# Performance work log

Hardware: AMD Instinct MI355X
Metric: run time of the kernel (lower is better)

## Reference

```python
import jax, jax.numpy as jnp
import numpy as np

# ---- box encoding helpers ----

def _cv2_corners(b):
    # b: [..., 5] (cx, cy, w, h, angle) -> [..., 4, 2] rotated-rect vertices
    cx, cy, w, h, a = (b[..., i] for i in range(5))
    c, s = jnp.cos(a), jnp.sin(a)
    dx, dy = w * 0.5, h * 0.5
    lx = jnp.stack([-dx, dx, dx, -dx], axis=-1)   # [..., 4]
    ly = jnp.stack([-dy, -dy, dy, dy], axis=-1)
    x = cx[..., None] + lx * c[..., None] - ly * s[..., None]
    y = cy[..., None] + lx * s[..., None] + ly * c[..., None]
    return jnp.stack([x, y], axis=-1)


def _vertices_to_cv2(v):
    # v: [..., 4, 2] ordered vertices -> [..., 5] (cx, cy, w, h, angle)
    ctr = v.mean(axis=-2)
    e1 = v[..., 1, :] - v[..., 0, :]
    e2 = v[..., 3, :] - v[..., 0, :]
    w = jnp.linalg.norm(e1, axis=-1)
    h = jnp.linalg.norm(e2, axis=-1)
    ang = jnp.arctan2(e1[..., 1], e1[..., 0])
    return jnp.concatenate([ctr, w[..., None], h[..., None], ang[..., None]], axis=-1)


def _corners_to_hbb(corners):
    # [..., 4, 2] -> [..., 4] (x1, y1, x2, y2)
    return jnp.concatenate([corners.min(axis=-2), corners.max(axis=-2)], axis=-1)


def _box_iou(a, b):
    # a: [B, N, 4], b: [B, M, 4] -> [B, N, M] axis-aligned IoU
    lt = jnp.maximum(a[:, :, None, :2], b[:, None, :, :2])
    rb = jnp.minimum(a[:, :, None, 2:], b[:, None, :, 2:])
    wh = jnp.clip(rb - lt, 0.0)
    inter = wh[..., 0] * wh[..., 1]
    area_a = (a[..., 2] - a[..., 0]) * (a[..., 3] - a[..., 1])
    area_b = (b[..., 2] - b[..., 0]) * (b[..., 3] - b[..., 1])
    union = area_a[:, :, None] + area_b[:, None, :] - inter
    return inter / jnp.clip(union, 1e-7)


def setup_inputs() -> dict:
    key = jax.random.key(0)
    ks = jax.random.split(key, 6)
    B, N, M, C = 8, 16384, 128, 81

    def rand_boxes(k, shape):
        k1, k2, k3 = jax.random.split(k, 3)
        ctr = jax.random.uniform(k1, shape + (2,), minval=0.0, maxval=1000.0)
        wh = jax.random.uniform(k2, shape + (2,), minval=16.0, maxval=160.0)
        ang = jax.random.uniform(k3, shape + (1,), minval=-1.5, maxval=1.5)
        return jnp.concatenate([ctr, wh, ang], axis=-1)

    box_pred = rand_boxes(ks[0], (B, N))
    gt = rand_boxes(ks[1], (B, M))
    # seed the first M predictions near the GT so positives (IoU>=0.5) exist
    box_pred = box_pred.at[:, :M].set(gt + 2.0 * jax.random.normal(ks[2], gt.shape))
    regression_targets = _cv2_corners(gt)                     # [B, M, 4, 2] vertices
    classification_targets = jax.random.randint(ks[3], (B, M), 0, C - 1)
    class_pred = jax.random.normal(ks[4], (B, N, C))
    return {
        "box_pred": box_pred,
        "class_pred": class_pred,
        "regression_targets": regression_targets,
        "classification_targets": classification_targets,
        "n_samples": 256,
    }


def reference(box_pred, class_pred, regression_targets, classification_targets, n_samples):
    B = box_pred.shape[0]
    C = class_pred.shape[-1]
    background_cls = C - 1
    k_pos = n_samples // 2
    k_neg = n_samples - k_pos

    box_targets_cv2 = _vertices_to_cv2(regression_targets)           # [B, M, 5]
    hbb_pred = _corners_to_hbb(_cv2_corners(box_pred))               # [B, N, 4]
    hbb_tgt = _corners_to_hbb(regression_targets)                    # [B, M, 4]
    iou = _box_iou(hbb_pred, hbb_tgt)                                # [B, N, M]

    def per_image(iou_i, labels_i, logits_i, boxp_i, boxt_i):
        max_iou = iou_i.max(axis=-1)                                 # [N]
        match = iou_i.argmax(axis=-1)                                # [N] matched GT idx
        pos_mask = max_iou >= 0.5
        # sample up to k_pos positives (highest IoU) and k_neg negatives (lowest IoU)
        pos_score = jnp.where(pos_mask, max_iou, -1.0)
        _, pos_idx = jax.lax.top_k(pos_score, k_pos)
        pos_valid = pos_mask[pos_idx]
        neg_score = jnp.where(pos_mask, -jnp.inf, -max_iou)
        _, neg_idx = jax.lax.top_k(neg_score, k_neg)
        neg_valid = ~pos_mask[neg_idx]
        # classification targets: matched GT label for positives, background otherwise
        cls_target = jnp.where(pos_mask, labels_i[match], background_cls)
        sel_idx = jnp.concatenate([pos_idx, neg_idx])                # [n_samples]
        sel_valid = jnp.concatenate([pos_valid, neg_valid])
        logp = jax.nn.log_softmax(logits_i[sel_idx], axis=-1)        # [n_samples, C]
        nll = -jnp.take_along_axis(logp, cls_target[sel_idx][:, None], axis=1)[:, 0]
        cls_loss = jnp.sum(nll * sel_valid.astype(logp.dtype))
        rel_pred = boxp_i[pos_idx]                                   # [k_pos, 5]
        rel_gt = boxt_i[match[pos_idx]]                              # [k_pos, 5]
        d = jnp.abs(rel_pred - rel_gt)
        sl1 = jnp.where(d < 1.0, 0.5 * d * d, d - 0.5)
        regr_loss = jnp.sum(sl1 * pos_valid[:, None].astype(sl1.dtype))
        return cls_loss, regr_loss

    cls_l, reg_l = jax.vmap(per_image)(
        iou, classification_targets, class_pred, box_pred, box_targets_cv2
    )
    classification_loss = cls_l.sum() / B
    regression_loss = reg_l.sum() / B
    total_loss = classification_loss + regression_loss
    return total_loss, classification_loss, regression_loss
```

## Files before the change

kernel.cpp:

```cpp
#include <hip/hip_runtime.h>
#include <math.h>

#define B_ 8
#define N_ 16384
#define M_ 128
#define C_ 81
#define TPB 512
#define KPT 32
#define NWAVE (TPB / 64)
#define ABLK 32
#define ATPB 512

__global__ __launch_bounds__(ATPB)
void iou_fused(const float* __restrict__ bp,
               const float* __restrict__ rt,
               unsigned* __restrict__ poskey,
               unsigned* __restrict__ negkey,
               unsigned char* __restrict__ match8,
               unsigned* __restrict__ cnt,
               float* __restrict__ out) {
    __shared__ float sx1[M_], sy1[M_], sx2[M_], sy2[M_], sab[M_];
    __shared__ unsigned scnt[ATPB / 64];
    int b = blockIdx.y;
    int n = blockIdx.x * ATPB + threadIdx.x;

    if (blockIdx.x == 0 && blockIdx.y == 0 && threadIdx.x < 3)
        out[threadIdx.x] = 0.0f;

    if (threadIdx.x < M_) {
        const float* v = rt + ((size_t)b * M_ + threadIdx.x) * 8;
        float x0 = v[0], y0 = v[1], x1 = v[2], y1 = v[3];
        float x2 = v[4], y2 = v[5], x3 = v[6], y3 = v[7];
        float mnx = fminf(fminf(x0, x1), fminf(x2, x3));
        float mny = fminf(fminf(y0, y1), fminf(y2, y3));
        float mxx = fmaxf(fmaxf(x0, x1), fmaxf(x2, x3));
        float mxy = fmaxf(fmaxf(y0, y1), fmaxf(y2, y3));
        sx1[threadIdx.x] = mnx; sy1[threadIdx.x] = mny;
        sx2[threadIdx.x] = mxx; sy2[threadIdx.x] = mxy;
        sab[threadIdx.x] = (mxx - mnx) * (mxy - mny);
    }
    __syncthreads();

    const float* p = bp + ((size_t)b * N_ + n) * 5;
    float cx = p[0], cy = p[1], w = p[2], h = p[3], a = p[4];
    float c = cosf(a), s = sinf(a);
    float dx = w * 0.5f, dy = h * 0.5f;
    float ex = fabsf(dx * c) + fabsf(dy * s);
    float ey = fabsf(dx * s) + fabsf(dy * c);
    float ax1 = cx - ex, ay1 = cy - ey, ax2 = cx + ex, ay2 = cy + ey;
    float area_a = (ax2 - ax1) * (ay2 - ay1);

    float bin = -1.0f, bun = 1.0f;
    int bm = 0;
#pragma unroll 4
    for (int m = 0; m < M_; m++) {
        float lx = fmaxf(ax1, sx1[m]), ly = fmaxf(ay1, sy1[m]);
        float rx = fminf(ax2, sx2[m]), ry = fminf(ay2, sy2[m]);
        float ww = fmaxf(rx - lx, 0.0f), hh = fmaxf(ry - ly, 0.0f);
        float inter = ww * hh;
        float uni = area_a + sab[m] - inter;
        bool better = inter * bun > bin * uni;
        bin = better ? inter : bin;
        bun = better ? uni : bun;
        bm = better ? m : bm;
    }
    float iou = bin / bun;
    unsigned bits = __float_as_uint(iou);
    bool pos = (iou >= 0.5f);
    size_t gi = (size_t)b * N_ + n;
    poskey[gi] = pos ? ~(bits | 0x80000000u) : 0xFFFFFFFFu;
    negkey[gi] = pos ? 0xFFFFFFFFu : (bits | 0x80000000u);
    match8[gi] = (unsigned char)bm;

    unsigned posb = (unsigned)__popcll(__ballot(pos));
    unsigned zerb = (unsigned)__popcll(__ballot(bits == 0u));
    int lane = threadIdx.x & 63, wv = threadIdx.x >> 6;
    if (lane == 0) scnt[wv] = posb | (zerb << 16);
    __syncthreads();
    if (threadIdx.x == 0) {
        unsigned t = 0;
#pragma unroll
        for (int i = 0; i < ATPB / 64; i++) t += scnt[i];
        cnt[(size_t)b * ABLK + blockIdx.x] = t;
    }
}

__device__ __forceinline__ unsigned wave_sum6(unsigned c) {
    unsigned s = 0;
#pragma unroll
    for (int bit = 0; bit < 6; bit++)
        s += (unsigned)__popcll(__ballot((c >> bit) & 1u)) << bit;
    return s;
}

__device__ __forceinline__ unsigned bsum(unsigned c, unsigned* slot) {
    unsigned ws = wave_sum6(c);
    if ((threadIdx.x & 63) == 0) slot[threadIdx.x >> 6] = ws;
    __syncthreads();
    unsigned r = 0;
#pragma unroll
    for (int i = 0; i < NWAVE; i++) r += slot[i];
    return r;
}

__global__ __launch_bounds__(TPB)
void select_loss(const unsigned* __restrict__ keys_pos,
                 const unsigned* __restrict__ keys_neg,
                 const unsigned char* __restrict__ match8,
                 const float* __restrict__ logits, const float* __restrict__ bp,
                 const float* __restrict__ rt, const int* __restrict__ labels,
                 const int* __restrict__ ns_ptr, const unsigned* __restrict__ cnt,
                 float* __restrict__ out) {
    int type = blockIdx.x;
    int b = blockIdx.y;
    __shared__ float s_cv2[5][M_];
    __shared__ unsigned red[2 * NWAVE] __attribute__((aligned(16)));
    __shared__ float fredc[NWAVE], fredr[NWAVE];
    __shared__ unsigned sel[256];
    __shared__ unsigned selcnt;
    __shared__ unsigned s_tot;

    int tid = threadIdx.x;
    int lane = tid & 63, wv = tid >> 6;
    if (tid == 0) selcnt = 0;

    const unsigned* kb = (type == 0) ? keys_pos : keys_neg;
    const uint4* k4 = (const uint4*)(kb + (size_t)b * N_);
    uint4 kv[KPT / 4];
#pragma unroll
    for (int q = 0; q < KPT / 4; q++) kv[q] = k4[tid * (KPT / 4) + q];

    if (type == 0 && tid < M_) {
        const float* v = rt + ((size_t)b * M_ + tid) * 8;
        float x0 = v[0], y0 = v[1], x1 = v[2], y1 = v[3];
        float x2 = v[4], y2 = v[5], x3 = v[6], y3 = v[7];
        s_cv2[0][tid] = (x0 + x1 + x2 + x3) * 0.25f;
        s_cv2[1][tid] = (y0 + y1 + y2 + y3) * 0.25f;
        float e1x = x1 - x0, e1y = y1 - y0;
        float e2x = x3 - x0, e2y = y3 - y0;
        s_cv2[2][tid] = sqrtf(e1x * e1x + e1y * e1y);
        s_cv2[3][tid] = sqrtf(e2x * e2x + e2y * e2y);
        s_cv2[4][tid] = atan2f(e1y, e1x);
    }

    if (wv == 0) {
        unsigned c = (lane < ABLK) ? cnt[(size_t)b * ABLK + lane] : 0u;
#pragma unroll
        for (int o = 1; o < 64; o <<= 1) c += __shfl_xor(c, o);
        if (lane == 0) s_tot = c;
    }

    int ns = ns_ptr[0];
    unsigned ktar = (type == 0) ? (unsigned)(ns / 2) : (unsigned)(ns - ns / 2);
    if (ktar > 256u) ktar = 256u;

    unsigned key[KPT];
#pragma unroll
    for (int q = 0; q < KPT / 4; q++) {
        key[q * 4 + 0] = kv[q].x; key[q * 4 + 1] = kv[q].y;
        key[q * 4 + 2] = kv[q].z; key[q * 4 + 3] = kv[q].w;
    }
    int base = tid * KPT;

    __syncthreads();

    unsigned tot = s_tot;
    unsigned pos_total = tot & 0xFFFFu;
    unsigned zero_total = tot >> 16;
    unsigned V = (type == 0) ? pos_total : (unsigned)N_ - pos_total;
    unsigned keff = (ktar < V) ? ktar : V;

    int pc = 0;
    if (keff == V) {
#pragma unroll
        for (int j = 0; j < KPT; j++) {
            if (key[j] != 0xFFFFFFFFu) {
                unsigned p = atomicAdd(&selcnt, 1u);
                sel[p] = (unsigned)(base + j);
            }
        }
    } else {
        unsigned Ckey, m;
        bool zshort = (type == 1) && (zero_total >= keff);
        if (zshort) {
            Ckey = 0x80000000u;
            m = 0u;
        } else {
            unsigned lo = (type == 0) ? 0x40000000u : 0x80000000u;
            unsigned hi = (type == 0) ? 0x41000000u : 0xC0000000u;
            while (lo < hi) {
                unsigned mid = lo + ((hi - lo) >> 1);
                unsigned c = 0;
#pragma unroll
                for (int j = 0; j < KPT; j++) c += (key[j] <= mid) ? 1u : 0u;
                unsigned t2 = bsum(c, red + NWAVE * ((pc++) & 1));
                if (t2 >= keff) hi = mid; else lo = mid + 1;
            }
            Ckey = lo;
            unsigned cl = 0;
#pragma unroll
            for (int j = 0; j < KPT; j++) cl += (key[j] < Ckey) ? 1u : 0u;
            m = bsum(cl, red + NWAVE * ((pc++) & 1));
        }
        unsigned e = keff - m;

        unsigned ce = 0;
#pragma unroll
        for (int j = 0; j < KPT; j++) ce += (key[j] == Ckey) ? 1u : 0u;

        unsigned sc = ce;
#pragma unroll
        for (int o = 1; o < 64; o <<= 1) {
            unsigned t = __shfl_up(sc, o);
            if (lane >= o) sc += t;
        }
        unsigned* slot = red + NWAVE * ((pc++) & 1);
        if (lane == 63) slot[wv] = sc;
        __syncthreads();
        unsigned off = 0;
        for (int i = 0; i < wv; i++) off += slot[i];
        unsigned rank = off + sc - ce;

#pragma unroll
        for (int j = 0; j < KPT; j++) {
            unsigned k = key[j];
            bool s = false;
            if (k < Ckey) s = true;
            else if (k == Ckey) { s = (rank < e); rank++; }
            if (s) {
                unsigned p = atomicAdd(&selcnt, 1u);
                sel[p] = (unsigned)(base + j);
            }
        }
    }
    __syncthreads();
    unsigned total_sel = selcnt;

    float cls_sum = 0.f, reg_sum = 0.f;
    int q = tid & 3;
    for (unsigned sm = (unsigned)(tid >> 2); sm < total_sel; sm += TPB / 4) {
        unsigned i = sel[sm];
        const float* row = logits + ((size_t)b * N_ + i) * C_;
        int c0 = q * 21;
        int c1 = (c0 + 21 < C_) ? c0 + 21 : C_;
        float mx = -INFINITY;
        for (int c = c0; c < c1; c++) mx = fmaxf(mx, row[c]);
        mx = fmaxf(mx, __shfl_xor(mx, 1));
        mx = fmaxf(mx, __shfl_xor(mx, 2));
        float se = 0.f;
        for (int c = c0; c < c1; c++) se += expf(row[c] - mx);
        se += __shfl_xor(se, 1);
        se += __shfl_xor(se, 2);
        if (q == 0) {
            float lse = mx + logf(se);
            if (type == 0) {
                int g_gt = (int)match8[(size_t)b * N_ + i];
                int tc = labels[b * M_ + g_gt];
                cls_sum += lse - row[tc];
                const float* pp = bp + ((size_t)b * N_ + i) * 5;
#pragma unroll
                for (int d = 0; d < 5; d++) {
                    float ad = fabsf(pp[d] - s_cv2[d][g_gt]);
                    reg_sum += (ad < 1.f) ? 0.5f * ad * ad : ad - 0.5f;
                }
            } else {
                cls_sum += lse - row[C_ - 1];
            }
        }
    }

#pragma unroll
    for (int o = 32; o; o >>= 1) {
        cls_sum += __shfl_down(cls_sum, o);
        reg_sum += __shfl_down(reg_sum, o);
    }
    if (lane == 0) { fredc[wv] = cls_sum; fredr[wv] = reg_sum; }
    __syncthreads();
    if (tid == 0) {
        float cs = 0.f, rs = 0.f;
#pragma unroll
        for (int i = 0; i < NWAVE; i++) { cs += fredc[i]; rs += fredr[i]; }
        const float invB = 1.0f / (float)B_;
        atomicAdd(&out[0], (cs + rs) * invB);
        atomicAdd(&out[1], cs * invB);
        atomicAdd(&out[2], rs * invB);
    }
}

extern "C" void kernel_launch(void* const* d_in, const int* in_sizes, int n_in,
                              void* d_out, int out_size, void* d_ws, size_t ws_size,
                              hipStream_t stream) {
    const float* box_pred = (const float*)d_in[0];
    const float* class_pred = (const float*)d_in[1];
    const float* reg_tgt = (const float*)d_in[2];
    const int* cls_tgt = (const int*)d_in[3];
    const int* n_samples = (const int*)d_in[4];

    unsigned* poskey = (unsigned*)d_ws;
    unsigned* negkey = poskey + (size_t)B_ * N_;
    unsigned* cnt = negkey + (size_t)B_ * N_;
    unsigned char* match8 = (unsigned char*)(cnt + B_ * ABLK);
    float* out = (float*)d_out;

    iou_fused<<<dim3(ABLK, B_), ATPB, 0, stream>>>(box_pred, reg_tgt, poskey,
                                                   negkey, match8, cnt, out);
    select_loss<<<dim3(2, B_), TPB, 0, stream>>>(poskey, negkey, match8,
                                                 class_pred, box_pred, reg_tgt,
                                                 cls_tgt, n_samples, cnt, out);
}
```

Baseline: 125.8 us.

## Vectorize IoU shared loads, double select block size, replace atomics with prefix-scan compaction

The IoU loop now reads the GT box arrays from shared memory as float4, four boxes at a time. The select kernel doubles threads per block, which halves the keys each thread holds. Its selection replaces shared-memory atomicAdd compaction with a packed prefix scan that counts below-threshold and tie keys together, so each thread writes its selected indices to a deterministic offset. This removes atomic contention and one extra block reduction, and the ordering becomes deterministic. The larger block may raise register pressure and synchronisation cost.

Result: slower. 129.2 us (+2.7%).

```diff
diff --git a/kernel.cpp b/kernel.cpp
--- a/kernel.cpp
+++ b/kernel.cpp
@@ -5,8 +5,8 @@
 #define N_ 16384
 #define M_ 128
 #define C_ 81
-#define TPB 512
-#define KPT 32
+#define TPB 1024
+#define KPT (N_ / TPB)
 #define NWAVE (TPB / 64)
 #define ABLK 32
 #define ATPB 512
@@ -19,7 +19,7 @@
                unsigned char* __restrict__ match8,
                unsigned* __restrict__ cnt,
                float* __restrict__ out) {
-    __shared__ float sx1[M_], sy1[M_], sx2[M_], sy2[M_], sab[M_];
+    __shared__ __align__(16) float sx1[M_], sy1[M_], sx2[M_], sy2[M_], sab[M_];
     __shared__ unsigned scnt[ATPB / 64];
     int b = blockIdx.y;
     int n = blockIdx.x * ATPB + threadIdx.x;
@@ -50,19 +50,33 @@
     float ax1 = cx - ex, ay1 = cy - ey, ax2 = cx + ex, ay2 = cy + ey;
     float area_a = (ax2 - ax1) * (ay2 - ay1);
 
+    const float4* X1 = (const float4*)sx1;
+    const float4* Y1 = (const float4*)sy1;
+    const float4* X2 = (const float4*)sx2;
+    const float4* Y2 = (const float4*)sy2;
+    const float4* AB = (const float4*)sab;
     float bin = -1.0f, bun = 1.0f;
     int bm = 0;
-#pragma unroll 4
-    for (int m = 0; m < M_; m++) {
-        float lx = fmaxf(ax1, sx1[m]), ly = fmaxf(ay1, sy1[m]);
-        float rx = fminf(ax2, sx2[m]), ry = fminf(ay2, sy2[m]);
-        float ww = fmaxf(rx - lx, 0.0f), hh = fmaxf(ry - ly, 0.0f);
-        float inter = ww * hh;
-        float uni = area_a + sab[m] - inter;
-        bool better = inter * bun > bin * uni;
-        bin = better ? inter : bin;
-        bun = better ? uni : bun;
-        bm = better ? m : bm;
+#pragma unroll 2
+    for (int m4 = 0; m4 < M_ / 4; m4++) {
+        float4 qx1 = X1[m4], qy1 = Y1[m4], qx2 = X2[m4], qy2 = Y2[m4], qab = AB[m4];
+        const float bx1[4] = {qx1.x, qx1.y, qx1.z, qx1.w};
+        const float by1[4] = {qy1.x, qy1.y, qy1.z, qy1.w};
+        const float bx2[4] = {qx2.x, qx2.y, qx2.z, qx2.w};
+        const float by2[4] = {qy2.x, qy2.y, qy2.z, qy2.w};
+        const float bab[4] = {qab.x, qab.y, qab.z, qab.w};
+#pragma unroll
+        for (int j = 0; j < 4; j++) {
+            float lx = fmaxf(ax1, bx1[j]), ly = fmaxf(ay1, by1[j]);
+            float rx = fminf(ax2, bx2[j]), ry = fminf(ay2, by2[j]);
+            float ww = fmaxf(rx - lx, 0.0f), hh = fmaxf(ry - ly, 0.0f);
+            float inter = ww * hh;
+            float uni = area_a + bab[j] - inter;
+            bool better = inter * bun > bin * uni;
+            bin = better ? inter : bin;
+            bun = better ? uni : bun;
+            bm = better ? (m4 * 4 + j) : bm;
+        }
     }
     float iou = bin / bun;
     unsigned bits = __float_as_uint(iou);
@@ -117,12 +131,10 @@
     __shared__ unsigned red[2 * NWAVE] __attribute__((aligned(16)));
     __shared__ float fredc[NWAVE], fredr[NWAVE];
     __shared__ unsigned sel[256];
-    __shared__ unsigned selcnt;
     __shared__ unsigned s_tot;
 
     int tid = threadIdx.x;
     int lane = tid & 63, wv = tid >> 6;
-    if (tid == 0) selcnt = 0;
 
     const unsigned* kb = (type == 0) ? keys_pos : keys_neg;
     const uint4* k4 = (const uint4*)(kb + (size_t)b * N_);
@@ -170,71 +182,69 @@
     unsigned V = (type == 0) ? pos_total : (unsigned)N_ - pos_total;
     unsigned keff = (ktar < V) ? ktar : V;
 
+    unsigned Ckey;
     int pc = 0;
     if (keff == V) {
-#pragma unroll
-        for (int j = 0; j < KPT; j++) {
-            if (key[j] != 0xFFFFFFFFu) {
-                unsigned p = atomicAdd(&selcnt, 1u);
-                sel[p] = (unsigned)(base + j);
-            }
+        Ckey = 0xFFFFFFFFu;
+    } else if (type == 1 && zero_total >= keff) {
+        Ckey = 0x80000000u;
+    } else {
+        unsigned lo = (type == 0) ? 0x40000000u : 0x80000000u;
+        unsigned hi = (type == 0) ? 0x41000000u : 0xC0000000u;
+        while (lo < hi) {
+            unsigned mid = lo + ((hi - lo) >> 1);
+            unsigned c = 0;
+#pragma unroll
+            for (int j = 0; j < KPT; j++) c += (key[j] <= mid) ? 1u : 0u;
+            unsigned t2 = bsum(c, red + NWAVE * ((pc++) & 1));
+            if (t2 >= keff) hi = mid; else lo = mid + 1;
         }
-    } else {
-        unsigned Ckey, m;
-        bool zshort = (type == 1) && (zero_total >= keff);
-        if (zshort) {
-            Ckey = 0x80000000u;
-            m = 0u;
-        } else {
-            unsigned lo = (type == 0) ? 0x40000000u : 0x80000000u;
-            unsigned hi = (type == 0) ? 0x41000000u : 0xC0000000u;
-            while (lo < hi) {
-                unsigned mid = lo + ((hi - lo) >> 1);
-                unsigned c = 0;
-#pragma unroll
-                for (int j = 0; j < KPT; j++) c += (key[j] <= mid) ? 1u : 0u;
-                unsigned t2 = bsum(c, red + NWAVE * ((pc++) & 1));
-                if (t2 >= keff) hi = mid; else lo = mid + 1;
-            }
-            Ckey = lo;
-            unsigned cl = 0;
-#pragma unroll
-            for (int j = 0; j < KPT; j++) cl += (key[j] < Ckey) ? 1u : 0u;
-            m = bsum(cl, red + NWAVE * ((pc++) & 1));
+        Ckey = lo;
+    }
+
+    unsigned cl = 0, ce = 0;
+#pragma unroll
+    for (int j = 0; j < KPT; j++) {
+        cl += (key[j] < Ckey) ? 1u : 0u;
+        ce += (key[j] == Ckey) ? 1u : 0u;
+    }
+    unsigned pk = cl | (ce << 16);
+    unsigned sc = pk;
+#pragma unroll
+    for (int o = 1; o < 64; o <<= 1) {
+        unsigned t = __shfl_up(sc, o);
+        if (lane >= o) sc += t;
+    }
+    unsigned* slot = red + NWAVE * ((pc++) & 1);
+    if (lane == 63) slot[wv] = sc;
+    __syncthreads();
+    unsigned off = 0, wtot = 0;
+#pragma unroll
+    for (int i = 0; i < NWAVE; i++) {
+        unsigned sv = slot[i];
+        off += (i < wv) ? sv : 0u;
+        wtot += sv;
+    }
+    unsigned excl = off + sc - pk;
+    unsigned cl_excl = excl & 0xFFFFu;
+    unsigned ce_excl = excl >> 16;
+    unsigned m = wtot & 0xFFFFu;
+    unsigned e = keff - m;
+
+    unsigned wbase = cl_excl + ((ce_excl < e) ? ce_excl : e);
+    unsigned tie_r = ce_excl;
+#pragma unroll
+    for (int j = 0; j < KPT; j++) {
+        unsigned k = key[j];
+        if (k < Ckey) {
+            sel[wbase++] = (unsigned)(base + j);
+        } else if (k == Ckey) {
+            if (tie_r < e) sel[wbase++] = (unsigned)(base + j);
+            tie_r++;
         }
-        unsigned e = keff - m;
-
-        unsigned ce = 0;
-#pragma unroll
-        for (int j = 0; j < KPT; j++) ce += (key[j] == Ckey) ? 1u : 0u;
-
-        unsigned sc = ce;
-#pragma unroll
-        for (int o = 1; o < 64; o <<= 1) {
-            unsigned t = __shfl_up(sc, o);
-            if (lane >= o) sc += t;
-        }
-        unsigned* slot = red + NWAVE * ((pc++) & 1);
-        if (lane == 63) slot[wv] = sc;
-        __syncthreads();
-        unsigned off = 0;
-        for (int i = 0; i < wv; i++) off += slot[i];
-        unsigned rank = off + sc - ce;
-
-#pragma unroll
-        for (int j = 0; j < KPT; j++) {
-            unsigned k = key[j];
-            bool s = false;
-            if (k < Ckey) s = true;
-            else if (k == Ckey) { s = (rank < e); rank++; }
-            if (s) {
-                unsigned p = atomicAdd(&selcnt, 1u);
-                sel[p] = (unsigned)(base + j);
-            }
-        }
-    }
-    __syncthreads();
-    unsigned total_sel = selcnt;
+    }
+    __syncthreads();
+    unsigned total_sel = keff;
 
     float cls_sum = 0.f, reg_sum = 0.f;
     int q = tid & 3;
```
